# Optimization experiments

Hardware: AMD Instinct MI355X
Metric: run time of the kernel (lower is better)

## Reference

```python
import jax, jax.numpy as jnp
import numpy as np

G, N0, E0 = 10000, 32, 64          # graphs, nodes/graph, edges/graph
NF, NEF, H, D = 64, 64, 128, 256   # num_features, num_edge_features, nhid, ddi_nhid
B = 4096                           # ddi batch_size (pos edges; neg edges follow)
NEG_DECAY = 0.5
RATIO = 0.5


def _lin(k, fan_in, shape):
    s = 1.0 / np.sqrt(fan_in)
    return jax.random.uniform(k, shape, jnp.float32, -s, s)


def setup_inputs() -> dict:
    key = jax.random.key(0)
    ks = jax.random.split(key, 40)
    N, E = G * N0, G * E0
    x = jax.random.normal(ks[0], (N, NF), jnp.float32)
    off = jnp.repeat(jnp.arange(G, dtype=jnp.int32) * N0, E0)
    edge_src = off + jax.random.randint(ks[1], (E,), 0, N0, jnp.int32)
    edge_dst = off + jax.random.randint(ks[2], (E,), 0, N0, jnp.int32)
    edge_weight = jax.random.uniform(ks[3], (E,), jnp.float32)
    ddi_edge_index = jax.random.randint(ks[4], (2, 2 * B), 0, G, jnp.int32)
    ddi_edge_attr = jax.random.normal(ks[5], (2 * B, NEF), jnp.float32)
    p = {}
    p['W1'] = _lin(ks[6], NF, (NF, H)); p['b1'] = jnp.zeros((H,), jnp.float32)
    p['Ws1r'] = _lin(ks[7], H, (H, 1)); p['Ws1n'] = _lin(ks[8], H, (H, 1)); p['bs1'] = jnp.zeros((1,), jnp.float32)
    p['W2'] = _lin(ks[9], H, (H, H)); p['b2'] = jnp.zeros((H,), jnp.float32)
    p['Ws2r'] = _lin(ks[10], H, (H, 1)); p['Ws2n'] = _lin(ks[11], H, (H, 1)); p['bs2'] = jnp.zeros((1,), jnp.float32)
    p['W3'] = _lin(ks[12], H, (H, H)); p['b3'] = jnp.zeros((H,), jnp.float32)
    p['Ws3r'] = _lin(ks[13], H, (H, 1)); p['Ws3n'] = _lin(ks[14], H, (H, 1)); p['bs3'] = jnp.zeros((1,), jnp.float32)
    p['Wd'] = _lin(ks[15], 6 * H, (6 * H, D)); p['bd'] = jnp.zeros((D,), jnp.float32)
    p['Wl1'] = _lin(ks[16], D, (D, D)); p['bl1'] = _lin(ks[17], D, (D,))
    p['Wl2'] = _lin(ks[18], D, (D, D)); p['bl2'] = _lin(ks[19], D, (D,))
    p['Wl3'] = _lin(ks[20], NEF, (NEF, D)); p['bl3'] = _lin(ks[21], NEF, (D,))
    return dict(x=x, edge_src=edge_src, edge_dst=edge_dst, edge_weight=edge_weight,
                ddi_edge_index=ddi_edge_index, ddi_edge_attr=ddi_edge_attr, **p)


def gcn(x, src, dst, ew, W, b):
    # PyG GCNConv: add self-loops (weight 1), symmetric normalization, sum-aggregate
    h = x @ W                                              # [N, out]
    deg = jnp.zeros(x.shape[0], x.dtype).at[dst].add(ew) + 1.0
    dis = jax.lax.rsqrt(deg)
    norm = dis[src] * ew * dis[dst]                        # [E]
    out = jnp.zeros_like(h).at[dst].add(norm[:, None] * h[src])
    out = out + (dis * dis)[:, None] * h                   # self-loop term
    return out + b


def sag_pool(x, src, dst, ew, Wr, Wn, bn, n_per_graph):
    # SAGPooling: score = tanh(GraphConv(x)); keep top ceil(ratio*n) nodes per graph
    N, Hd = x.shape
    g = N // n_per_graph
    agg = jnp.zeros((N, Hd), x.dtype).at[dst].add(ew[:, None] * x[src])
    score = jnp.tanh((agg @ Wn + bn + x @ Wr)[:, 0])       # [N]
    k = int(np.ceil(RATIO * n_per_graph))
    topv, topi = jax.lax.top_k(score.reshape(g, n_per_graph), k)   # [g, k]
    perm = (jnp.arange(g, dtype=jnp.int32)[:, None] * n_per_graph + topi.astype(jnp.int32)).reshape(-1)
    xk = x[perm] * topv.reshape(-1)[:, None]               # gate kept nodes by score
    old2new = jnp.full((N,), -1, jnp.int32).at[perm].set(jnp.arange(g * k, dtype=jnp.int32))
    ns, nd = old2new[src], old2new[dst]
    valid = (ns >= 0) & (nd >= 0)
    new_ew = jnp.where(valid, ew, 0.0)                     # zero-weight == filtered edge
    ns = jnp.where(valid, ns, 0)
    nd = jnp.where(valid, nd, 0)
    return xk, ns, nd, new_ew, k


def readout(x, k):
    # gmp || gap with contiguous, equal-size graphs
    xg = x.reshape(-1, k, x.shape[1])
    return jnp.concatenate([xg.max(axis=1), xg.mean(axis=1)], axis=1)


def reference(x, edge_src, edge_dst, edge_weight, ddi_edge_index, ddi_edge_attr,
              W1, b1, Ws1r, Ws1n, bs1, W2, b2, Ws2r, Ws2n, bs2,
              W3, b3, Ws3r, Ws3n, bs3, Wd, bd, Wl1, bl1, Wl2, bl2, Wl3, bl3):
    h = jax.nn.relu(gcn(x, edge_src, edge_dst, edge_weight, W1, b1))
    h, s, d, ew, k1 = sag_pool(h, edge_src, edge_dst, edge_weight, Ws1r, Ws1n, bs1, N0)
    x1 = readout(h, k1)
    h = jax.nn.relu(gcn(h, s, d, ew, W2, b2))
    h, s, d, ew, k2 = sag_pool(h, s, d, ew, Ws2r, Ws2n, bs2, k1)
    x2 = readout(h, k2)
    h = jax.nn.relu(gcn(h, s, d, ew, W3, b3))
    h, s, d, ew, k3 = sag_pool(h, s, d, ew, Ws3r, Ws3n, bs3, k2)
    x3 = readout(h, k3)
    feat = jnp.concatenate([x1, x2, x3], axis=1)           # [G, 6H] drug features
    # dropout_ratio=0.0 (eval): identity
    ds, dd = ddi_edge_index[0], ddi_edge_index[1]
    dew = jnp.ones(ds.shape, feat.dtype)
    z = jax.nn.relu(gcn(feat, ds, dd, dew, Wd, bd))        # [G, D]
    src_f, tgt_f = z[ds], z[dd]
    pos_x = jax.nn.sigmoid(src_f[:B] @ Wl1 + bl1)
    pos_y = jax.nn.sigmoid(tgt_f[:B] @ Wl2 + bl2)
    neg_x = jax.nn.sigmoid(src_f[B:] @ Wl1 + bl1)
    neg_y = jax.nn.sigmoid(tgt_f[B:] @ Wl2 + bl2)
    pos_a = jax.nn.sigmoid(ddi_edge_attr[:B] @ Wl3 + bl3)
    neg_a = jax.nn.sigmoid(ddi_edge_attr[B:] @ Wl3 + bl3)
    lp = pos_x + pos_a - pos_y
    ln = neg_x + neg_a - neg_y
    norm_pos = jnp.linalg.norm(lp, axis=1)
    norm_neg = jnp.linalg.norm(ln, axis=1)
    loss = 2.0 * D - norm_pos + NEG_DECAY * norm_neg
    return loss, norm_pos, norm_neg, pos_x
```

## Files before the change

### kernel.cpp

```cpp
#include <hip/hip_runtime.h>
#include <math.h>

#define GG   10000
#define NN0  32
#define EE0  64
#define NFF  64
#define HH   128
#define DD   256
#define BB   4096
#define E2B  8192
#define SIXH 768
#define APAD 36

typedef unsigned short u16;
typedef __attribute__((ext_vector_type(8))) short short8v;
typedef __attribute__((ext_vector_type(4))) short short4v;
typedef __attribute__((ext_vector_type(4))) float f32x4;

static __device__ __forceinline__ u16 f2bf(float x) {
  unsigned u = __float_as_uint(x);
  return (u16)((u + 0x7FFFu + ((u >> 16) & 1u)) >> 16);
}
static __device__ __forceinline__ float bf2f(u16 h) {
  return __uint_as_float(((unsigned)h) << 16);
}


template<int M, int KK, int K, int SX, bool IND, bool LAST>
__device__ __forceinline__ void stage(
    const float* __restrict__ Wg, const float* __restrict__ bg,
    const float* __restrict__ Wr, const float* __restrict__ Wn, const float* __restrict__ bs,
    float* bufX, float* bufY, float* s_A,
    float* s_dis, float* s_cm, float* s_sc2,
    float* s_v1, float* s_v2, float* s_score, int* s_rank, int* s_inv,
    int& src_r, int& dst_r, float& ew_r,
    u16* __restrict__ featg, int t)
{
  if (t < EE0)
    atomicAdd(&s_A[dst_r*APAD + src_r], ew_r);
  __syncthreads();

  if (t < M) {
    float deg = 1.f;
#pragma unroll
    for (int m0 = 0; m0 < M; m0 += 4) {
      const float4 a4 = *(const float4*)(s_A + t*APAD + m0);
      deg += a4.x + a4.y + a4.z + a4.w;
    }
    const float dis = rsqrtf(deg);
    const float gg = IND ? s_score[s_inv[t]] : 1.f;
    s_dis[t] = dis; s_cm[t] = dis*gg; s_sc2[t] = dis*dis*gg;
  }
  __syncthreads();

  {
    constexpr int CGB = K/4, RGB = 256/CGB, R = M/RGB;
    const int cg = t % CGB, rg = t / CGB;
    const int c0 = cg * 4;
    float acc[R][4];
#pragma unroll
    for (int i = 0; i < R; ++i) { acc[i][0]=0.f; acc[i][1]=0.f; acc[i][2]=0.f; acc[i][3]=0.f; }
#pragma unroll 2
    for (int m0 = 0; m0 < M; m0 += 4) {
      float4 a[R];
#pragma unroll
      for (int i = 0; i < R; ++i)
        a[i] = *(const float4*)(s_A + (rg*R + i)*APAD + m0);
#pragma unroll
      for (int j = 0; j < 4; ++j) {
        const int m = m0 + j;
        const int row = IND ? s_inv[m] : m;
        const float4 xv = *(const float4*)(bufX + row*SX + c0);
        const float cmm = s_cm[m];
#pragma unroll
        for (int i = 0; i < R; ++i) {
          const float aj = (j==0) ? a[i].x : (j==1) ? a[i].y : (j==2) ? a[i].z : a[i].w;
          const float cf = aj * cmm;
          acc[i][0] = fmaf(cf, xv.x, acc[i][0]);
          acc[i][1] = fmaf(cf, xv.y, acc[i][1]);
          acc[i][2] = fmaf(cf, xv.z, acc[i][2]);
          acc[i][3] = fmaf(cf, xv.w, acc[i][3]);
        }
      }
    }
#pragma unroll
    for (int i = 0; i < R; ++i) {
      const int r = rg*R + i;
      const int rr = IND ? s_inv[r] : r;
      const float4 xv = *(const float4*)(bufX + rr*SX + c0);
      const float dr = s_dis[r], sc = s_sc2[r];
      float4 v;
      v.x = fmaf(sc, xv.x, acc[i][0]*dr);
      v.y = fmaf(sc, xv.y, acc[i][1]*dr);
      v.z = fmaf(sc, xv.z, acc[i][2]*dr);
      v.w = fmaf(sc, xv.w, acc[i][3]*dr);
      *(float4*)(bufY + r*K + c0) = v;
    }
  }
  __syncthreads();

  if constexpr (K != HH) {
    constexpr int R = M / 4;
    const int cg = t & 63;
    const int rg = t >> 6;
    float acc0[R], acc1[R];
#pragma unroll
    for (int i = 0; i < R; ++i) { acc0[i]=0.f; acc1[i]=0.f; }
#pragma unroll 2
    for (int k0 = 0; k0 < K; k0 += 4) {
      float4 yv[R];
#pragma unroll
      for (int i = 0; i < R; ++i)
        yv[i] = *(const float4*)(bufY + (rg*R + i)*K + k0);
#pragma unroll
      for (int j = 0; j < 4; ++j) {
        const float2 w = *(const float2*)(Wg + (size_t)(k0+j)*HH + cg*2);
#pragma unroll
        for (int i = 0; i < R; ++i) {
          const float yj = (j==0) ? yv[i].x : (j==1) ? yv[i].y : (j==2) ? yv[i].z : yv[i].w;
          acc0[i] = fmaf(yj, w.x, acc0[i]);
          acc1[i] = fmaf(yj, w.y, acc1[i]);
        }
      }
    }
    const float2 b2  = *(const float2*)(bg + cg*2);
    const float2 wn2 = *(const float2*)(Wn + cg*2);
    const float2 wr2 = *(const float2*)(Wr + cg*2);
#pragma unroll
    for (int i = 0; i < R; ++i) {
      const int row = rg*R + i;
      const float ox = fmaxf(acc0[i] + b2.x, 0.f);
      const float oy = fmaxf(acc1[i] + b2.y, 0.f);
      float2 v; v.x=ox; v.y=oy;
      *(float2*)(bufX + row*HH + cg*2) = v;
      float p1 = ox*wn2.x + oy*wn2.y;
      float p2 = ox*wr2.x + oy*wr2.y;
#pragma unroll
      for (int off = 32; off >= 1; off >>= 1) {
        p1 += __shfl_xor(p1, off);
        p2 += __shfl_xor(p2, off);
      }
      if ((t & 63) == 0) { s_v1[row] = p1; s_v2[row] = p2; }
    }
  } else {
    constexpr int R = M / 2;
    const int cg  = t & 63;
    const int sub = (t >> 6) & 1;
    const int pr  = t >> 7;
    const int kbase = pr * (K/2);
    float acc0[R], acc1[R];
#pragma unroll
    for (int i = 0; i < R; ++i) { acc0[i]=0.f; acc1[i]=0.f; }
#pragma unroll 2
    for (int k0 = 0; k0 < K/2; k0 += 4) {
      float4 yv[R];
#pragma unroll
      for (int i = 0; i < R; ++i)
        yv[i] = *(const float4*)(bufY + (sub*R + i)*K + kbase + k0);
#pragma unroll
      for (int j = 0; j < 4; ++j) {
        const float2 w = *(const float2*)(Wg + (size_t)(kbase+k0+j)*HH + cg*2);
#pragma unroll
        for (int i = 0; i < R; ++i) {
          const float yj = (j==0) ? yv[i].x : (j==1) ? yv[i].y : (j==2) ? yv[i].z : yv[i].w;
          acc0[i] = fmaf(yj, w.x, acc0[i]);
          acc1[i] = fmaf(yj, w.y, acc1[i]);
        }
      }
    }
    __syncthreads();
    float* pdst = pr ? bufY : bufX;
#pragma unroll
    for (int i = 0; i < R; ++i) {
      float2 v; v.x=acc0[i]; v.y=acc1[i];
      *(float2*)(pdst + (sub*R + i)*HH + cg*2) = v;
    }
    __syncthreads();
    constexpr int RE = M / 8;
    const int ecg = t & 31, erg = t >> 5;
    const int f0 = ecg * 4;
    const float4 b4  = *(const float4*)(bg + f0);
    const float4 wn4 = *(const float4*)(Wn + f0);
    const float4 wr4 = *(const float4*)(Wr + f0);
#pragma unroll
    for (int i = 0; i < RE; ++i) {
      const int row = erg*RE + i;
      const float4 p0 = *(const float4*)(bufX + row*HH + f0);
      const float4 p1v = *(const float4*)(bufY + row*HH + f0);
      const float ox = fmaxf(p0.x + p1v.x + b4.x, 0.f);
      const float oy = fmaxf(p0.y + p1v.y + b4.y, 0.f);
      const float oz = fmaxf(p0.z + p1v.z + b4.z, 0.f);
      const float ow = fmaxf(p0.w + p1v.w + b4.w, 0.f);
      float4 v; v.x=ox; v.y=oy; v.z=oz; v.w=ow;
      *(float4*)(bufX + row*HH + f0) = v;
      float p1 = ox*wn4.x + oy*wn4.y + oz*wn4.z + ow*wn4.w;
      float p2 = ox*wr4.x + oy*wr4.y + oz*wr4.z + ow*wr4.w;
#pragma unroll
      for (int off = 16; off >= 1; off >>= 1) {
        p1 += __shfl_xor(p1, off);
        p2 += __shfl_xor(p2, off);
      }
      if ((t & 31) == 0) { s_v1[row] = p1; s_v2[row] = p2; }
    }
  }
  __syncthreads();

  if (t < 64) {
    if (t < M) {
      float sc = bs[0] + s_v2[t];
#pragma unroll
      for (int m0 = 0; m0 < M; m0 += 4) {
        const float4 a4 = *(const float4*)(s_A  + t*APAD + m0);
        const float4 v4 = *(const float4*)(s_v1 + m0);
        sc += a4.x*v4.x + a4.y*v4.y + a4.z*v4.z + a4.w*v4.w;
      }
      s_score[t] = tanhf(sc);
    }
    if (t < M) {
      const float st = s_score[t];
      int r = 0;
      for (int m = 0; m < M; ++m) {
        const float sm = s_score[m];
        r += (sm > st) || (sm == st && m < t);
      }
      s_rank[t] = r;
      if (r < KK) s_inv[r] = t;
    }
    if (!LAST) {
      const int a = s_rank[src_r];
      const int b = s_rank[dst_r];
      const bool val = (a < KK) && (b < KK);
      ew_r  = val ? ew_r : 0.f;
      src_r = val ? a : 0;
      dst_r = val ? b : 0;
    }
  }
  __syncthreads();

  {
    const int f = t & 127, which = t >> 7;
    float r_acc = which ? 0.f : -INFINITY;
#pragma unroll
    for (int r = 0; r < KK; ++r) {
      const int n = s_inv[r];
      const float v = bufX[n*HH + f] * s_score[n];
      r_acc = which ? (r_acc + v) : fmaxf(r_acc, v);
    }
    featg[which*HH + f] = f2bf(which ? r_acc * (1.f/KK) : r_acc);
  }
  if (!LAST) {
    for (int idx = t; idx < NN0*APAD/4; idx += 256) {
      float4 z4; z4.x = 0.f; z4.y = 0.f; z4.z = 0.f; z4.w = 0.f;
      *(float4*)(s_A + idx*4) = z4;
    }
  }
  __syncthreads();
}

__global__ __launch_bounds__(256, 5) void graph_kernel(
    const float* __restrict__ x,
    const int* __restrict__ esrc, const int* __restrict__ edst, const float* __restrict__ ewg,
    const float* __restrict__ W1, const float* __restrict__ b1,
    const float* __restrict__ Ws1r, const float* __restrict__ Ws1n, const float* __restrict__ bs1,
    const float* __restrict__ W2, const float* __restrict__ b2,
    const float* __restrict__ Ws2r, const float* __restrict__ Ws2n, const float* __restrict__ bs2,
    const float* __restrict__ W3, const float* __restrict__ b3,
    const float* __restrict__ Ws3r, const float* __restrict__ Ws3n, const float* __restrict__ bs3,
    u16* __restrict__ featB)
{
  __shared__ __align__(16) float bufX[NN0*HH];
  __shared__ __align__(16) float bufY[2048];
  __shared__ __align__(16) float s_A[NN0*APAD];
  __shared__ __align__(16) float s_dis[NN0], s_cm[NN0], s_sc2[NN0];
  __shared__ __align__(16) float s_v1[NN0], s_v2[NN0], s_score[NN0];
  __shared__ __align__(16) int   s_rank[NN0], s_inv[NN0];

  const int t = threadIdx.x;
  const int g = blockIdx.x;

  for (int idx = t; idx < NN0*NFF/4; idx += 256)
    *(float4*)(bufX + idx*4) = *(const float4*)(x + (size_t)g*NN0*NFF + idx*4);
  int src_r, dst_r; float ew_r;
  {
    const int e = g*EE0 + (t & 63);
    src_r = esrc[e] - g*NN0;
    dst_r = edst[e] - g*NN0;
    ew_r  = ewg[e];
  }
  for (int idx = t; idx < NN0*APAD/4; idx += 256) {
    float4 z4; z4.x = 0.f; z4.y = 0.f; z4.z = 0.f; z4.w = 0.f;
    *(float4*)(s_A + idx*4) = z4;
  }
  __syncthreads();

  u16* featg = featB + (size_t)g * SIXH;

  stage<NN0, 16, NFF, NFF, false, false>(W1, b1, Ws1r, Ws1n, bs1,
      bufX, bufY, s_A, s_dis, s_cm, s_sc2, s_v1, s_v2, s_score, s_rank, s_inv,
      src_r, dst_r, ew_r, featg, t);
  stage<16, 8, HH, HH, true, false>(W2, b2, Ws2r, Ws2n, bs2,
      bufX, bufY, s_A, s_dis, s_cm, s_sc2, s_v1, s_v2, s_score, s_rank, s_inv,
      src_r, dst_r, ew_r, featg + 256, t);
  stage<8, 4, HH, HH, true, true>(W3, b3, Ws3r, Ws3n, bs3,
      bufX, bufY, s_A, s_dis, s_cm, s_sc2, s_v1, s_v2, s_score, s_rank, s_inv,
      src_r, dst_r, ew_r, featg + 512, t);
}


__global__ void k_convW(const float* __restrict__ Wd,
                        const float* __restrict__ Wl1, const float* __restrict__ Wl2,
                        u16* __restrict__ WdT, u16* __restrict__ WlT)
{
  const int b = blockIdx.x, t = threadIdx.x;
  if (b < 256) {
#pragma unroll
    for (int i = 0; i < 3; ++i) {
      const int k = i*256 + t;
      WdT[(size_t)b*SIXH + k] = f2bf(Wd[(size_t)k*DD + b]);
    }
  } else {
    const int c = b - 256;
    const float* src = (c < 256) ? Wl1 : Wl2;
    WlT[(size_t)c*DD + t] = f2bf(src[(size_t)t*DD + (c & 255)]);
  }
}

__global__ void k_deg_init(float* __restrict__ degf) {
  int i = blockIdx.x*256 + threadIdx.x;
  if (i < GG) degf[i] = 1.f;
}

__global__ void k_deg_acc(const int* __restrict__ ddi, float* __restrict__ degf) {
  int e = blockIdx.x*256 + threadIdx.x;
  if (e < E2B) atomicAdd(&degf[ddi[E2B + e]], 1.f);
}

__global__ __launch_bounds__(256) void k_ddi_mfma(const u16* __restrict__ featB,
    const u16* __restrict__ WdT, const float* __restrict__ degf,
    const float* __restrict__ bd, float* __restrict__ hdd, float* __restrict__ z)
{
  const int t = threadIdx.x;
  const int l = t & 63, w = t >> 6;
  const int r0 = blockIdx.x * 16;
  const int l15 = l & 15, kb = l >> 4;
  const int c0 = w * 64;
  f32x4 acc[4];
#pragma unroll
  for (int fi = 0; fi < 4; ++fi) { acc[fi][0]=0.f; acc[fi][1]=0.f; acc[fi][2]=0.f; acc[fi][3]=0.f; }
  const u16* aptr = featB + (size_t)(r0 + l15)*SIXH + kb*8;
#pragma unroll 2
  for (int kk = 0; kk < SIXH; kk += 32) {
    const short8v a = *(const short8v*)(aptr + kk);
#pragma unroll
    for (int fi = 0; fi < 4; ++fi) {
      const short8v b = *(const short8v*)(WdT + (size_t)(c0 + fi*16 + l15)*SIXH + kk + kb*8);
      acc[fi] = __builtin_amdgcn_mfma_f32_16x16x32_bf16(a, b, acc[fi], 0, 0, 0);
    }
  }
#pragma unroll
  for (int j = 0; j < 4; ++j) {
    const int gr = r0 + kb*4 + j;
    const float rd = 1.f / degf[gr];
#pragma unroll
    for (int fi = 0; fi < 4; ++fi) {
      const int c = c0 + fi*16 + l15;
      const float v = acc[fi][j];
      hdd[(size_t)gr*DD + c] = v;
      z[(size_t)gr*DD + c] = fmaf(v, rd, bd[c]);
    }
  }
}

__global__ void k_scatter(const int* __restrict__ ddi, const float* __restrict__ degf,
                          const float* __restrict__ hdd, float* __restrict__ z)
{
  const int t = threadIdx.x;
#pragma unroll
  for (int j = 0; j < 4; ++j) {
    const int e = blockIdx.x*4 + j;
    const int s = ddi[e], d = ddi[E2B + e];
    const float nrm = rsqrtf(degf[s]) * rsqrtf(degf[d]);
    atomicAdd(&z[(size_t)d*DD + t], nrm * hdd[(size_t)s*DD + t]);
  }
}

__global__ void k_zsplit(const float* __restrict__ z,
                         u16* __restrict__ zh, u16* __restrict__ zl)
{
  const int i4 = blockIdx.x*256 + threadIdx.x;
  const float4 v = *(const float4*)(z + (size_t)i4*4);
  short4v h, lo;
  {
    const u16 h0 = f2bf(v.x); h[0] = (short)h0; lo[0] = (short)f2bf(v.x - bf2f(h0));
    const u16 h1 = f2bf(v.y); h[1] = (short)h1; lo[1] = (short)f2bf(v.y - bf2f(h1));
    const u16 h2 = f2bf(v.z); h[2] = (short)h2; lo[2] = (short)f2bf(v.z - bf2f(h2));
    const u16 h3 = f2bf(v.w); h[3] = (short)h3; lo[3] = (short)f2bf(v.w - bf2f(h3));
  }
  *(short4v*)(zh + (size_t)i4*4) = h;
  *(short4v*)(zl + (size_t)i4*4) = lo;
}

__global__ __launch_bounds__(256) void k_xy_mfma(const u16* __restrict__ zh,
    const u16* __restrict__ zl, const u16* __restrict__ WlT,
    const float* __restrict__ bl1, const float* __restrict__ bl2,
    float* __restrict__ X, float* __restrict__ Y)
{
  const int t = threadIdx.x;
  const int l = t & 63, w = t >> 6;
  const int r0 = blockIdx.x * 16;
  const int l15 = l & 15, kb = l >> 4;
  const int c0 = w * 128;
  f32x4 acc[8];
#pragma unroll
  for (int fi = 0; fi < 8; ++fi) { acc[fi][0]=0.f; acc[fi][1]=0.f; acc[fi][2]=0.f; acc[fi][3]=0.f; }
  const u16* ah = zh + (size_t)(r0 + l15)*DD + kb*8;
  const u16* al = zl + (size_t)(r0 + l15)*DD + kb*8;
#pragma unroll 1
  for (int kk = 0; kk < DD; kk += 32) {
    const short8v a0 = *(const short8v*)(ah + kk);
    const short8v a1 = *(const short8v*)(al + kk);
#pragma unroll
    for (int fi = 0; fi < 8; ++fi) {
      const short8v b = *(const short8v*)(WlT + (size_t)(c0 + fi*16 + l15)*DD + kk + kb*8);
      acc[fi] = __builtin_amdgcn_mfma_f32_16x16x32_bf16(a0, b, acc[fi], 0, 0, 0);
      acc[fi] = __builtin_amdgcn_mfma_f32_16x16x32_bf16(a1, b, acc[fi], 0, 0, 0);
    }
  }
#pragma unroll
  for (int fi = 0; fi < 8; ++fi) {
    const int cg = c0 + fi*16 + l15;
    float* dst = (cg < 256) ? X : Y;
    const float bias = (cg < 256) ? bl1[cg] : bl2[cg - 256];
    const int c = cg & 255;
#pragma unroll
    for (int j = 0; j < 4; ++j) {
      const int gr = r0 + kb*4 + j;
      dst[(size_t)gr*DD + c] = 1.f / (1.f + expf(-(acc[fi][j] + bias)));
    }
  }
}

__global__ __launch_bounds__(256) void k_edge(const float* __restrict__ X,
    const float* __restrict__ Y, const int* __restrict__ ddi,
    const float* __restrict__ attr,
    const float* __restrict__ Wl3, const float* __restrict__ bl3,
    float* __restrict__ out)
{
  __shared__ __align__(16) float s_a[8*68];
  __shared__ __align__(16) float s_r[8*257];
  const int t = threadIdx.x;
  const int e0 = blockIdx.x * 8;
  for (int idx = t; idx < 8*64; idx += 256) {
    const int r = idx >> 6, k = idx & 63;
    s_a[r*68 + k] = attr[(size_t)(e0 + r)*NFF + k];
  }
  __syncthreads();
  float acc[8];
#pragma unroll
  for (int r = 0; r < 8; ++r) acc[r] = bl3[t];
#pragma unroll 4
  for (int k = 0; k < 64; ++k) {
    const float w = Wl3[(size_t)k*DD + t];
#pragma unroll
    for (int r = 0; r < 8; ++r) acc[r] = fmaf(s_a[r*68 + k], w, acc[r]);
  }
#pragma unroll
  for (int r = 0; r < 8; ++r) {
    const int e = e0 + r;
    const int s = ddi[e], d = ddi[E2B + e];
    const float xv = X[(size_t)s*DD + t];
    const float yv = Y[(size_t)d*DD + t];
    const float av = 1.f / (1.f + expf(-acc[r]));
    const float lp = xv + av - yv;
    s_r[r*257 + t] = lp * lp;
    if (e < BB) out[12288 + (size_t)e*DD + t] = xv;
  }
  __syncthreads();
  {
    const int row = t >> 5, l = t & 31;
    float s = 0.f;
#pragma unroll
    for (int j = 0; j < 8; ++j) s += s_r[row*257 + l + 32*j];
#pragma unroll
    for (int off = 16; off >= 1; off >>= 1) s += __shfl_xor(s, off);
    if (l == 0) {
      const float nrm = sqrtf(s);
      const int e = e0 + row;
      if (e < BB) out[4096 + e] = nrm;
      else        out[8192 + (e - BB)] = nrm;
    }
  }
}

__global__ void k_loss(float* __restrict__ out) {
  int i = blockIdx.x*256 + threadIdx.x;
  if (i < BB) out[i] = 2.f*(float)DD - out[4096 + i] + 0.5f*out[8192 + i];
}


extern "C" void kernel_launch(void* const* d_in, const int* in_sizes, int n_in,
                              void* d_out, int out_size, void* d_ws, size_t ws_size,
                              hipStream_t stream)
{
  const float* x    = (const float*)d_in[0];
  const int*   esrc = (const int*)d_in[1];
  const int*   edst = (const int*)d_in[2];
  const float* ewt  = (const float*)d_in[3];
  const int*   ddi  = (const int*)d_in[4];
  const float* attr = (const float*)d_in[5];
  const float* W1   = (const float*)d_in[6];  const float* b1  = (const float*)d_in[7];
  const float* Ws1r = (const float*)d_in[8];  const float* Ws1n= (const float*)d_in[9];  const float* bs1 = (const float*)d_in[10];
  const float* W2   = (const float*)d_in[11]; const float* b2  = (const float*)d_in[12];
  const float* Ws2r = (const float*)d_in[13]; const float* Ws2n= (const float*)d_in[14]; const float* bs2 = (const float*)d_in[15];
  const float* W3   = (const float*)d_in[16]; const float* b3  = (const float*)d_in[17];
  const float* Ws3r = (const float*)d_in[18]; const float* Ws3n= (const float*)d_in[19]; const float* bs3 = (const float*)d_in[20];
  const float* Wd   = (const float*)d_in[21]; const float* bd  = (const float*)d_in[22];
  const float* Wl1  = (const float*)d_in[23]; const float* bl1 = (const float*)d_in[24];
  const float* Wl2  = (const float*)d_in[25]; const float* bl2 = (const float*)d_in[26];
  const float* Wl3  = (const float*)d_in[27]; const float* bl3 = (const float*)d_in[28];

  float* ws = (float*)d_ws;
  u16*  featB = (u16*)ws;
  float* hdd  = ws + 3840000;
  float* zb   = hdd + (size_t)GG*DD;
  float* degf = zb  + (size_t)GG*DD;
  u16*  zh    = (u16*)(degf + GG);
  u16*  zl    = zh + (size_t)GG*DD;
  u16*  WdT   = zl + (size_t)GG*DD;
  u16*  WlT   = WdT + 256*SIXH;
  float* Xb   = ws;
  float* Yb   = hdd;
  float* out  = (float*)d_out;

  k_convW<<<768, 256, 0, stream>>>(Wd, Wl1, Wl2, WdT, WlT);
  graph_kernel<<<GG, 256, 0, stream>>>(x, esrc, edst, ewt,
      W1, b1, Ws1r, Ws1n, bs1, W2, b2, Ws2r, Ws2n, bs2, W3, b3, Ws3r, Ws3n, bs3, featB);
  k_deg_init<<<(GG + 255)/256, 256, 0, stream>>>(degf);
  k_deg_acc<<<(E2B + 255)/256, 256, 0, stream>>>(ddi, degf);
  k_ddi_mfma<<<GG/16, 256, 0, stream>>>(featB, WdT, degf, bd, hdd, zb);
  k_scatter<<<E2B/4, 256, 0, stream>>>(ddi, degf, hdd, zb);
  k_zsplit<<<GG*DD/4/256, 256, 0, stream>>>(zb, zh, zl);
  k_xy_mfma<<<GG/16, 256, 0, stream>>>(zh, zl, WlT, bl1, bl2, Xb, Yb);
  k_edge<<<E2B/8, 256, 0, stream>>>(Xb, Yb, ddi, attr, Wl3, bl3, out);
  k_loss<<<(BB + 255)/256, 256, 0, stream>>>(out);
}
```

Before: 433.4 us.

## Use split-fp16 MFMA for per-graph GCN weight matmuls

Replaces the scalar FP32 FMA matmuls inside the per-graph stage with 16x16x32 fp16 MFMA instructions. Each operand is split into a high fp16 part and a scaled low residual, and three MFMAs per step keep close to FP32 accuracy. A new pre-kernel transposes W1/W2/W3 and splits them into fp16 hi/lo copies. The score projections are now reduced per wave into partial slots and summed later. The cost is extra conversion work and three times the MFMA count, plus a small added accuracy risk from the fp16 split.

Result: faster. 373.3 us (-13.9%).

```diff
diff --git a/kernel.cpp b/kernel.cpp
--- a/kernel.cpp
+++ b/kernel.cpp
@@ -16,6 +16,8 @@
 typedef __attribute__((ext_vector_type(8))) short short8v;
 typedef __attribute__((ext_vector_type(4))) short short4v;
 typedef __attribute__((ext_vector_type(4))) float f32x4;
+typedef _Float16 h8f __attribute__((ext_vector_type(8)));
+typedef _Float16 h4f __attribute__((ext_vector_type(4)));
 
 static __device__ __forceinline__ u16 f2bf(float x) {
   unsigned u = __float_as_uint(x);
@@ -28,14 +30,21 @@
 
 template<int M, int KK, int K, int SX, bool IND, bool LAST>
 __device__ __forceinline__ void stage(
-    const float* __restrict__ Wg, const float* __restrict__ bg,
+    const _Float16* __restrict__ WTh, const _Float16* __restrict__ WTl,
+    const float* __restrict__ bg,
     const float* __restrict__ Wr, const float* __restrict__ Wn, const float* __restrict__ bs,
-    float* bufX, float* bufY, float* s_A,
+    float* bufX, _Float16* ybh, _Float16* ybl, float* s_A,
     float* s_dis, float* s_cm, float* s_sc2,
-    float* s_v1, float* s_v2, float* s_score, int* s_rank, int* s_inv,
+    float* s_v1p, float* s_v2p, float* s_score, int* s_rank, int* s_inv,
     int& src_r, int& dst_r, float& ew_r,
     u16* __restrict__ featg, int t)
 {
+  constexpr int KP = K + 8;
+  constexpr int RT  = (M > 16) ? 2 : 1;
+  constexpr int CTW = (RT == 2) ? 4 : 2;
+  constexpr int KF  = K / 32;
+  constexpr int NS  = (RT == 2) ? 2 : 4;
+
   if (t < EE0)
     atomicAdd(&s_A[dst_r*APAD + src_r], ew_r);
   __syncthreads();
@@ -94,124 +103,91 @@
       v.y = fmaf(sc, xv.y, acc[i][1]*dr);
       v.z = fmaf(sc, xv.z, acc[i][2]*dr);
       v.w = fmaf(sc, xv.w, acc[i][3]*dr);
-      *(float4*)(bufY + r*K + c0) = v;
-    }
-  }
-  __syncthreads();
-
-  if constexpr (K != HH) {
-    constexpr int R = M / 4;
-    const int cg = t & 63;
-    const int rg = t >> 6;
-    float acc0[R], acc1[R];
-#pragma unroll
-    for (int i = 0; i < R; ++i) { acc0[i]=0.f; acc1[i]=0.f; }
-#pragma unroll 2
-    for (int k0 = 0; k0 < K; k0 += 4) {
-      float4 yv[R];
-#pragma unroll
-      for (int i = 0; i < R; ++i)
-        yv[i] = *(const float4*)(bufY + (rg*R + i)*K + k0);
+      h4f vh, vl;
+      _Float16 h;
+      h = (_Float16)v.x; vh[0] = h; vl[0] = (_Float16)((v.x - (float)h) * 2048.f);
+      h = (_Float16)v.y; vh[1] = h; vl[1] = (_Float16)((v.y - (float)h) * 2048.f);
+      h = (_Float16)v.z; vh[2] = h; vl[2] = (_Float16)((v.z - (float)h) * 2048.f);
+      h = (_Float16)v.w; vh[3] = h; vl[3] = (_Float16)((v.w - (float)h) * 2048.f);
+      *(h4f*)(ybh + r*KP + c0) = vh;
+      *(h4f*)(ybl + r*KP + c0) = vl;
+    }
+  }
+  __syncthreads();
+
+  {
+    const int l = t & 63, w = t >> 6;
+    const int l15 = l & 15, kb = l >> 4;
+    const int rt   = (RT == 2) ? (w >> 1) : 0;
+    const int ct0  = (RT == 2) ? ((w & 1) * CTW) : (w * CTW);
+    const int slot = (RT == 2) ? (w & 1) : w;
+
+    h8f ah[KF], al[KF];
+#pragma unroll
+    for (int kf = 0; kf < KF; ++kf) {
+      ah[kf] = *(const h8f*)(ybh + (rt*16 + l15)*KP + kf*32 + kb*8);
+      al[kf] = *(const h8f*)(ybl + (rt*16 + l15)*KP + kf*32 + kb*8);
+    }
+    float p1[4] = {0.f,0.f,0.f,0.f}, p2[4] = {0.f,0.f,0.f,0.f};
+#pragma unroll
+    for (int ci = 0; ci < CTW; ++ci) {
+      const int ct = ct0 + ci;
+      const int col = ct*16 + l15;
+      f32x4 a0 = {0.f,0.f,0.f,0.f}, a1 = {0.f,0.f,0.f,0.f};
+#pragma unroll
+      for (int kf = 0; kf < KF; ++kf) {
+        const h8f bh = *(const h8f*)(WTh + (size_t)col*K + kf*32 + kb*8);
+        const h8f bl = *(const h8f*)(WTl + (size_t)col*K + kf*32 + kb*8);
+        a0 = __builtin_amdgcn_mfma_f32_16x16x32_f16(ah[kf], bh, a0, 0, 0, 0);
+        a1 = __builtin_amdgcn_mfma_f32_16x16x32_f16(ah[kf], bl, a1, 0, 0, 0);
+        a1 = __builtin_amdgcn_mfma_f32_16x16x32_f16(al[kf], bh, a1, 0, 0, 0);
+      }
+      const float bb = bg[col], wnc = Wn[col], wrc = Wr[col];
 #pragma unroll
       for (int j = 0; j < 4; ++j) {
-        const float2 w = *(const float2*)(Wg + (size_t)(k0+j)*HH + cg*2);
-#pragma unroll
-        for (int i = 0; i < R; ++i) {
-          const float yj = (j==0) ? yv[i].x : (j==1) ? yv[i].y : (j==2) ? yv[i].z : yv[i].w;
-          acc0[i] = fmaf(yj, w.x, acc0[i]);
-          acc1[i] = fmaf(yj, w.y, acc1[i]);
-        }
-      }
-    }
-    const float2 b2  = *(const float2*)(bg + cg*2);
-    const float2 wn2 = *(const float2*)(Wn + cg*2);
-    const float2 wr2 = *(const float2*)(Wr + cg*2);
-#pragma unroll
-    for (int i = 0; i < R; ++i) {
-      const int row = rg*R + i;
-      const float ox = fmaxf(acc0[i] + b2.x, 0.f);
-      const float oy = fmaxf(acc1[i] + b2.y, 0.f);
-      float2 v; v.x=ox; v.y=oy;
-      *(float2*)(bufX + row*HH + cg*2) = v;
-      float p1 = ox*wn2.x + oy*wn2.y;
-      float p2 = ox*wr2.x + oy*wr2.y;
-#pragma unroll
-      for (int off = 32; off >= 1; off >>= 1) {
-        p1 += __shfl_xor(p1, off);
-        p2 += __shfl_xor(p2, off);
-      }
-      if ((t & 63) == 0) { s_v1[row] = p1; s_v2[row] = p2; }
-    }
-  } else {
-    constexpr int R = M / 2;
-    const int cg  = t & 63;
-    const int sub = (t >> 6) & 1;
-    const int pr  = t >> 7;
-    const int kbase = pr * (K/2);
-    float acc0[R], acc1[R];
-#pragma unroll
-    for (int i = 0; i < R; ++i) { acc0[i]=0.f; acc1[i]=0.f; }
-#pragma unroll 2
-    for (int k0 = 0; k0 < K/2; k0 += 4) {
-      float4 yv[R];
-#pragma unroll
-      for (int i = 0; i < R; ++i)
-        yv[i] = *(const float4*)(bufY + (sub*R + i)*K + kbase + k0);
+        const int row = rt*16 + kb*4 + j;
+        const float o = fmaxf(fmaf(a1[j], (1.f/2048.f), a0[j]) + bb, 0.f);
+        bufX[row*HH + col] = o;
+        p1[j] = fmaf(o, wnc, p1[j]);
+        p2[j] = fmaf(o, wrc, p2[j]);
+      }
+    }
+#pragma unroll
+    for (int j = 0; j < 4; ++j) {
+#pragma unroll
+      for (int off = 8; off >= 1; off >>= 1) {
+        p1[j] += __shfl_xor(p1[j], off);
+        p2[j] += __shfl_xor(p2[j], off);
+      }
+    }
+    if (l15 == 0) {
 #pragma unroll
       for (int j = 0; j < 4; ++j) {
-        const float2 w = *(const float2*)(Wg + (size_t)(kbase+k0+j)*HH + cg*2);
-#pragma unroll
-        for (int i = 0; i < R; ++i) {
-          const float yj = (j==0) ? yv[i].x : (j==1) ? yv[i].y : (j==2) ? yv[i].z : yv[i].w;
-          acc0[i] = fmaf(yj, w.x, acc0[i]);
-          acc1[i] = fmaf(yj, w.y, acc1[i]);
-        }
-      }
-    }
-    __syncthreads();
-    float* pdst = pr ? bufY : bufX;
-#pragma unroll
-    for (int i = 0; i < R; ++i) {
-      float2 v; v.x=acc0[i]; v.y=acc1[i];
-      *(float2*)(pdst + (sub*R + i)*HH + cg*2) = v;
-    }
-    __syncthreads();
-    constexpr int RE = M / 8;
-    const int ecg = t & 31, erg = t >> 5;
-    const int f0 = ecg * 4;
-    const float4 b4  = *(const float4*)(bg + f0);
-    const float4 wn4 = *(const float4*)(Wn + f0);
-    const float4 wr4 = *(const float4*)(Wr + f0);
-#pragma unroll
-    for (int i = 0; i < RE; ++i) {
-      const int row = erg*RE + i;
-      const float4 p0 = *(const float4*)(bufX + row*HH + f0);
-      const float4 p1v = *(const float4*)(bufY + row*HH + f0);
-      const float ox = fmaxf(p0.x + p1v.x + b4.x, 0.f);
-      const float oy = fmaxf(p0.y + p1v.y + b4.y, 0.f);
-      const float oz = fmaxf(p0.z + p1v.z + b4.z, 0.f);
-      const float ow = fmaxf(p0.w + p1v.w + b4.w, 0.f);
-      float4 v; v.x=ox; v.y=oy; v.z=oz; v.w=ow;
-      *(float4*)(bufX + row*HH + f0) = v;
-      float p1 = ox*wn4.x + oy*wn4.y + oz*wn4.z + ow*wn4.w;
-      float p2 = ox*wr4.x + oy*wr4.y + oz*wr4.z + ow*wr4.w;
-#pragma unroll
-      for (int off = 16; off >= 1; off >>= 1) {
-        p1 += __shfl_xor(p1, off);
-        p2 += __shfl_xor(p2, off);
-      }
-      if ((t & 31) == 0) { s_v1[row] = p1; s_v2[row] = p2; }
+        const int row = rt*16 + kb*4 + j;
+        s_v1p[slot*32 + row] = p1[j];
+        s_v2p[slot*32 + row] = p2[j];
+      }
     }
   }
   __syncthreads();
 
   if (t < 64) {
     if (t < M) {
-      float sc = bs[0] + s_v2[t];
+      float v2t = s_v2p[t] + s_v2p[32 + t];
+      if (NS == 4) v2t += s_v2p[64 + t] + s_v2p[96 + t];
+      float sc = bs[0] + v2t;
 #pragma unroll
       for (int m0 = 0; m0 < M; m0 += 4) {
-        const float4 a4 = *(const float4*)(s_A  + t*APAD + m0);
-        const float4 v4 = *(const float4*)(s_v1 + m0);
+        const float4 a4 = *(const float4*)(s_A + t*APAD + m0);
+        float4 v4 = *(const float4*)(s_v1p + m0);
+        const float4 vb = *(const float4*)(s_v1p + 32 + m0);
+        v4.x += vb.x; v4.y += vb.y; v4.z += vb.z; v4.w += vb.w;
+        if (NS == 4) {
+          const float4 vc = *(const float4*)(s_v1p + 64 + m0);
+          const float4 vd = *(const float4*)(s_v1p + 96 + m0);
+          v4.x += vc.x + vd.x; v4.y += vc.y + vd.y;
+          v4.z += vc.z + vd.z; v4.w += vc.w + vd.w;
+        }
         sc += a4.x*v4.x + a4.y*v4.y + a4.z*v4.z + a4.w*v4.w;
       }
       s_score[t] = tanhf(sc);
@@ -260,19 +236,20 @@
 __global__ __launch_bounds__(256, 5) void graph_kernel(
     const float* __restrict__ x,
     const int* __restrict__ esrc, const int* __restrict__ edst, const float* __restrict__ ewg,
-    const float* __restrict__ W1, const float* __restrict__ b1,
+    const _Float16* __restrict__ WT,
+    const float* __restrict__ b1,
     const float* __restrict__ Ws1r, const float* __restrict__ Ws1n, const float* __restrict__ bs1,
-    const float* __restrict__ W2, const float* __restrict__ b2,
+    const float* __restrict__ b2,
     const float* __restrict__ Ws2r, const float* __restrict__ Ws2n, const float* __restrict__ bs2,
-    const float* __restrict__ W3, const float* __restrict__ b3,
+    const float* __restrict__ b3,
     const float* __restrict__ Ws3r, const float* __restrict__ Ws3n, const float* __restrict__ bs3,
     u16* __restrict__ featB)
 {
   __shared__ __align__(16) float bufX[NN0*HH];
-  __shared__ __align__(16) float bufY[2048];
+  __shared__ __align__(16) _Float16 ybh[2304], ybl[2304];
   __shared__ __align__(16) float s_A[NN0*APAD];
-  __shared__ __align__(16) float s_dis[NN0], s_cm[NN0], s_sc2[NN0];
-  __shared__ __align__(16) float s_v1[NN0], s_v2[NN0], s_score[NN0];
+  __shared__ __align__(16) float s_dis[NN0], s_cm[NN0], s_sc2[NN0], s_score[NN0];
+  __shared__ __align__(16) float s_v1p[128], s_v2p[128];
   __shared__ __align__(16) int   s_rank[NN0], s_inv[NN0];
 
   const int t = threadIdx.x;
@@ -294,16 +271,53 @@
   __syncthreads();
 
   u16* featg = featB + (size_t)g * SIXH;
-
-  stage<NN0, 16, NFF, NFF, false, false>(W1, b1, Ws1r, Ws1n, bs1,
-      bufX, bufY, s_A, s_dis, s_cm, s_sc2, s_v1, s_v2, s_score, s_rank, s_inv,
+  const _Float16* W1h = WT;
+  const _Float16* W1l = W1h + 128*64;
+  const _Float16* W2h = W1l + 128*64;
+  const _Float16* W2l = W2h + 128*128;
+  const _Float16* W3h = W2l + 128*128;
+  const _Float16* W3l = W3h + 128*128;
+
+  stage<NN0, 16, NFF, NFF, false, false>(W1h, W1l, b1, Ws1r, Ws1n, bs1,
+      bufX, ybh, ybl, s_A, s_dis, s_cm, s_sc2, s_v1p, s_v2p, s_score, s_rank, s_inv,
       src_r, dst_r, ew_r, featg, t);
-  stage<16, 8, HH, HH, true, false>(W2, b2, Ws2r, Ws2n, bs2,
-      bufX, bufY, s_A, s_dis, s_cm, s_sc2, s_v1, s_v2, s_score, s_rank, s_inv,
+  stage<16, 8, HH, HH, true, false>(W2h, W2l, b2, Ws2r, Ws2n, bs2,
+      bufX, ybh, ybl, s_A, s_dis, s_cm, s_sc2, s_v1p, s_v2p, s_score, s_rank, s_inv,
       src_r, dst_r, ew_r, featg + 256, t);
-  stage<8, 4, HH, HH, true, true>(W3, b3, Ws3r, Ws3n, bs3,
-      bufX, bufY, s_A, s_dis, s_cm, s_sc2, s_v1, s_v2, s_score, s_rank, s_inv,
+  stage<8, 4, HH, HH, true, true>(W3h, W3l, b3, Ws3r, Ws3n, bs3,
+      bufX, ybh, ybl, s_A, s_dis, s_cm, s_sc2, s_v1p, s_v2p, s_score, s_rank, s_inv,
       src_r, dst_r, ew_r, featg + 512, t);
+}
+
+__global__ void k_convW123(const float* __restrict__ W1, const float* __restrict__ W2,
+                           const float* __restrict__ W3, _Float16* __restrict__ T)
+{
+  const int c = blockIdx.x;
+  const int k = threadIdx.x;
+  _Float16* W1h = T;
+  _Float16* W1l = W1h + 128*64;
+  _Float16* W2h = W1l + 128*64;
+  _Float16* W2l = W2h + 128*128;
+  _Float16* W3h = W2l + 128*128;
+  _Float16* W3l = W3h + 128*128;
+  if (k < 64) {
+    const float v = W1[(size_t)k*HH + c];
+    const _Float16 h = (_Float16)v;
+    W1h[c*64 + k] = h;
+    W1l[c*64 + k] = (_Float16)((v - (float)h) * 2048.f);
+  }
+  {
+    const float v = W2[(size_t)k*HH + c];
+    const _Float16 h = (_Float16)v;
+    W2h[c*HH + k] = h;
+    W2l[c*HH + k] = (_Float16)((v - (float)h) * 2048.f);
+  }
+  {
+    const float v = W3[(size_t)k*HH + c];
+    const _Float16 h = (_Float16)v;
+    W3h[c*HH + k] = h;
+    W3l[c*HH + k] = (_Float16)((v - (float)h) * 2048.f);
+  }
 }
 
 
@@ -528,13 +542,15 @@
   u16*  zl    = zh + (size_t)GG*DD;
   u16*  WdT   = zl + (size_t)GG*DD;
   u16*  WlT   = WdT + 256*SIXH;
+  _Float16* WgT = (_Float16*)(WlT + 512*DD);
   float* Xb   = ws;
   float* Yb   = hdd;
   float* out  = (float*)d_out;
 
   k_convW<<<768, 256, 0, stream>>>(Wd, Wl1, Wl2, WdT, WlT);
-  graph_kernel<<<GG, 256, 0, stream>>>(x, esrc, edst, ewt,
-      W1, b1, Ws1r, Ws1n, bs1, W2, b2, Ws2r, Ws2n, bs2, W3, b3, Ws3r, Ws3n, bs3, featB);
+  k_convW123<<<128, 128, 0, stream>>>(W1, W2, W3, WgT);
+  graph_kernel<<<GG, 256, 0, stream>>>(x, esrc, edst, ewt, WgT,
+      b1, Ws1r, Ws1n, bs1, b2, Ws2r, Ws2n, bs2, b3, Ws3r, Ws3n, bs3, featB);
   k_deg_init<<<(GG + 255)/256, 256, 0, stream>>>(degf);
   k_deg_acc<<<(E2B + 255)/256, 256, 0, stream>>>(ddi, degf);
   k_ddi_mfma<<<GG/16, 256, 0, stream>>>(featB, WdT, degf, bd, hdd, zb);
```
